# Optimization experiments

Hardware: AMD Instinct MI355X
Metric: run time of the kernel (lower is better)

Reference implementation:

```python
import jax, jax.numpy as jnp
import numpy as np

C = 256
HEADS = 8
HD = C // HEADS
EPS = 1e-5


def _layernorm(x, g, b):
    mu = jnp.mean(x, axis=-1, keepdims=True)
    var = jnp.var(x, axis=-1, keepdims=True)
    return (x - mu) * jax.lax.rsqrt(var + EPS) * g + b


def setup_inputs() -> dict:
    key = jax.random.key(0)
    ks = jax.random.split(key, 16)
    s = 0.02
    return {
        "x": jax.random.normal(ks[0], (1, C, 64, 64), jnp.float32),
        "bn_gamma": 1.0 + s * jax.random.normal(ks[1], (C,), jnp.float32),
        "bn_beta": s * jax.random.normal(ks[2], (C,), jnp.float32),
        "bn_mean": s * jax.random.normal(ks[3], (C,), jnp.float32),
        "bn_var": jnp.ones((C,), jnp.float32),
        "w_in": s * jax.random.normal(ks[4], (C, C), jnp.float32),
        "b_in": jnp.zeros((C,), jnp.float32),
        "ln1_g": jnp.ones((C,), jnp.float32),
        "ln1_b": jnp.zeros((C,), jnp.float32),
        "w_qkv": s * jax.random.normal(ks[5], (3 * C, C), jnp.float32),
        "b_qkv": jnp.zeros((3 * C,), jnp.float32),
        "w_ap": s * jax.random.normal(ks[6], (C, C), jnp.float32),
        "b_ap": jnp.zeros((C,), jnp.float32),
        "ln2_g": jnp.ones((C,), jnp.float32),
        "ln2_b": jnp.zeros((C,), jnp.float32),
        "w_ff1": s * jax.random.normal(ks[7], (4 * C, C), jnp.float32),
        "b_ff1": jnp.zeros((4 * C,), jnp.float32),
        "w_ff2": s * jax.random.normal(ks[8], (C, 4 * C), jnp.float32),
        "b_ff2": jnp.zeros((C,), jnp.float32),
        "w_out": s * jax.random.normal(ks[9], (C, C), jnp.float32),
        "b_out": jnp.zeros((C,), jnp.float32),
    }


def reference(x, bn_gamma, bn_beta, bn_mean, bn_var, w_in, b_in,
              ln1_g, ln1_b, w_qkv, b_qkv, w_ap, b_ap,
              ln2_g, ln2_b, w_ff1, b_ff1, w_ff2, b_ff2, w_out, b_out):
    b, c, h, w = x.shape
    t = h * w
    x_in = x
    # BatchNorm2d (eval mode: running stats)
    xn = (x - bn_mean[None, :, None, None]) * jax.lax.rsqrt(bn_var + EPS)[None, :, None, None]
    xn = xn * bn_gamma[None, :, None, None] + bn_beta[None, :, None, None]
    # proj_in 1x1 conv -> tokens [b, t, c]
    tok = xn.reshape(b, c, t).transpose(0, 2, 1)
    tok = tok @ w_in.T + b_in
    # transformer block (depth=1)
    y = _layernorm(tok, ln1_g, ln1_b)  # norm1
    qkv = y @ w_qkv.T + b_qkv  # [b, t, 3c], channel split (3, H, hd)
    qkv = qkv.reshape(b, t, 3, HEADS, HD)
    q = qkv[:, :, 0].transpose(0, 2, 1, 3)  # [b, H, t, hd]
    k = qkv[:, :, 1].transpose(0, 2, 1, 3)
    v = qkv[:, :, 2].transpose(0, 2, 1, 3)
    scale = HD ** (-0.5)
    attn = jax.nn.softmax(jnp.einsum('bhqd,bhkd->bhqk', q, k) * scale, axis=-1)
    o = jnp.einsum('bhqk,bhkd->bhqd', attn, v)  # [b, H, t, hd]
    o = o.transpose(0, 2, 1, 3).reshape(b, t, c)  # channels ordered (H, hd)
    o = o @ w_ap.T + b_ap  # attn proj 1x1
    attn_out = o + y  # VanillaAttention residual adds its (normed) input
    tok = tok + attn_out
    # FFN
    z = _layernorm(tok, ln2_g, ln2_b)
    z = jax.nn.gelu(z @ w_ff1.T + b_ff1, approximate=False)
    tok = tok + (z @ w_ff2.T + b_ff2)
    # back to image, proj_out 1x1, outer residual
    x4 = tok.transpose(0, 2, 1).reshape(b, c, h, w)
    out = jnp.einsum('oc,bchw->bohw', w_out, x4) + b_out[None, :, None, None]
    return out + x_in
```

## Files before the change

### kernel.cpp

```cpp
#include <hip/hip_runtime.h>
#include <math.h>

#define T_TOK 4096
#define C_DIM 256
#define EPSF  1e-5f
#define SC_QL (0.17677669529663687f * 1.4426950408889634f)

typedef short  bf16x8  __attribute__((ext_vector_type(8)));
typedef float  f32x4   __attribute__((ext_vector_type(4)));
typedef ushort ushort8 __attribute__((ext_vector_type(8)));

__device__ __forceinline__ short f2bf(float f) {
    unsigned u = __builtin_bit_cast(unsigned, f);
    unsigned r = (u + 0x7FFFu + ((u >> 16) & 1u)) >> 16;
    return (short)r;
}
__device__ __forceinline__ float bf2f(ushort u) {
    return __builtin_bit_cast(float, ((unsigned)u) << 16);
}
__device__ __forceinline__ unsigned pk_bf16(float a, float b) {
    const unsigned ua = __builtin_bit_cast(unsigned, a) + 0x8000u;
    const unsigned ub = __builtin_bit_cast(unsigned, b) + 0x8000u;
    return __builtin_amdgcn_perm(ub, ua, 0x07060302u);
}
template <int CTRL>
__device__ __forceinline__ float dppf(float x) {
    return __builtin_bit_cast(float,
        __builtin_amdgcn_mov_dpp(__builtin_bit_cast(int, x), CTRL, 0xF, 0xF, true));
}
__device__ __forceinline__ float rowsum16(float x) {
    x += dppf<0xB1>(x);
    x += dppf<0x4E>(x);
    x += dppf<0x141>(x);
    x += dppf<0x140>(x);
    return x;
}
#define MFMA16(a, b, c) __builtin_amdgcn_mfma_f32_16x16x32_bf16(a, b, c, 0, 0, 0)

__global__ __launch_bounds__(256) void prep_kernel(
    const float* __restrict__ w_in, const float* __restrict__ w_qkv,
    const float* __restrict__ w_ap, const float* __restrict__ w_ff1,
    const float* __restrict__ w_ff2, const float* __restrict__ w_out,
    const float* __restrict__ b_qkv, ushort* __restrict__ wbuf,
    float* __restrict__ bqs,
    const float* __restrict__ x, const float* __restrict__ gamma,
    const float* __restrict__ beta, const float* __restrict__ mean,
    const float* __restrict__ var, ushort* __restrict__ tin)
{
    __shared__ float tile[32][33];
    if (blockIdx.x < 896) {
        const int gid = blockIdx.x * 256 + threadIdx.x;
        const int e0 = gid * 4;
        const float* src; int off; float sc = 1.f;
        if (e0 < 65536)       { src = w_in;  off = e0; }
        else if (e0 < 262144) { src = w_qkv; off = e0 - 65536; if (off < 65536) sc = SC_QL; }
        else if (e0 < 327680) { src = w_ap;  off = e0 - 262144; }
        else if (e0 < 589824) { src = w_ff1; off = e0 - 327680; }
        else if (e0 < 851968) { src = w_ff2; off = e0 - 589824; }
        else                  { src = w_out; off = e0 - 851968; }
        const float4 v = *(const float4*)(src + off);
        ushort4 o;
        o.x = (ushort)f2bf(v.x * sc); o.y = (ushort)f2bf(v.y * sc);
        o.z = (ushort)f2bf(v.z * sc); o.w = (ushort)f2bf(v.w * sc);
        *(ushort4*)(wbuf + e0) = o;
        if (gid < 192) {
            const float s2 = (gid < 64) ? SC_QL : 1.f;
            float4 b = ((const float4*)b_qkv)[gid];
            b.x *= s2; b.y *= s2; b.z *= s2; b.w *= s2;
            ((float4*)bqs)[gid] = b;
        }
    } else {
        const int bidx = blockIdx.x - 896;
        const int t0 = (bidx & 127) * 32, c0 = (bidx >> 7) * 32;
        const int tx = threadIdx.x & 31, ty = threadIdx.x >> 5;
#pragma unroll
        for (int i = 0; i < 32; i += 8) {
            const int c = c0 + ty + i;
            const float a = rsqrtf(var[c] + EPSF) * gamma[c];
            const float d = beta[c] - mean[c] * a;
            tile[ty + i][tx] = x[c * T_TOK + t0 + tx] * a + d;
        }
        __syncthreads();
#pragma unroll
        for (int i = 0; i < 32; i += 8) {
            const int t = t0 + ty + i;
            tin[t * C_DIM + c0 + tx] = (ushort)f2bf(tile[tx][ty + i]);
        }
    }
}

__global__ __launch_bounds__(1024) void fused_pre(
    const ushort* __restrict__ tin, const ushort* __restrict__ wb_in,
    const float* __restrict__ b_in, const float* __restrict__ ln1_g,
    const float* __restrict__ ln1_b, const ushort* __restrict__ wb_qkv,
    const float* __restrict__ bqs, float* __restrict__ tok0,
    float* __restrict__ yout, ushort* __restrict__ qkvb)
{
    __shared__ ushort Atile[16 * 264];
    __shared__ ushort Ytile[16 * 264];
    __shared__ float  red[16][16][2];
    const int t0 = blockIdx.x * 16;
    const int tid = threadIdx.x, wv = tid >> 6, lane = tid & 63;
    const int c = lane & 15, g = lane >> 4;

    {
        const int r = tid >> 6, c0 = (tid & 63) * 4;
        *(ushort4*)&Atile[r * 264 + c0] = *(const ushort4*)(tin + (size_t)(t0 + r) * 256 + c0);
    }
    __syncthreads();

    f32x4 accp = {};
#pragma unroll
    for (int kc = 0; kc < 8; ++kc) {
        const bf16x8 af = *(const bf16x8*)&Atile[c * 264 + kc * 32 + g * 8];
        const bf16x8 bfv = *(const bf16x8*)(wb_in +
            (size_t)(wv * 16 + c) * 256 + kc * 32 + g * 8);
        accp = MFMA16(af, bfv, accp);
    }
    const int colp = wv * 16 + c;
    {
        const float bb = b_in[colp];
        float vs[4], s1[4], s2[4];
#pragma unroll
        for (int rr = 0; rr < 4; ++rr) {
            const float v = accp[rr] + bb;
            vs[rr] = v; s1[rr] = v; s2[rr] = v * v;
            tok0[(size_t)(t0 + 4 * g + rr) * 256 + colp] = v;
        }
#pragma unroll
        for (int rr = 0; rr < 4; ++rr) { s1[rr] = rowsum16(s1[rr]); s2[rr] = rowsum16(s2[rr]); }
        if (c == 0) {
#pragma unroll
            for (int rr = 0; rr < 4; ++rr) {
                red[wv][4 * g + rr][0] = s1[rr];
                red[wv][4 * g + rr][1] = s2[rr];
            }
        }
        __syncthreads();
        if (tid < 32) {
            const int row = tid >> 1, j = tid & 1;
            float s = 0.f;
#pragma unroll
            for (int w = 0; w < 16; ++w) s += red[w][row][j];
            red[0][row][j] = s;
        }
        __syncthreads();
        const float gg = ln1_g[colp], lb = ln1_b[colp];
#pragma unroll
        for (int rr = 0; rr < 4; ++rr) {
            const int row = 4 * g + rr;
            const float mu = red[0][row][0] * (1.0f / 256.0f);
            const float var = red[0][row][1] * (1.0f / 256.0f) - mu * mu;
            const float rs = rsqrtf(var + EPSF);
            const float yv = (vs[rr] - mu) * rs * gg + lb;
            yout[(size_t)(t0 + row) * 256 + colp] = yv;
            Ytile[row * 264 + colp] = (ushort)f2bf(yv);
        }
    }
    __syncthreads();

    f32x4 accq[3] = {};
#pragma unroll
    for (int kc = 0; kc < 8; ++kc) {
        const bf16x8 af = *(const bf16x8*)&Ytile[c * 264 + kc * 32 + g * 8];
#pragma unroll
        for (int nf = 0; nf < 3; ++nf) {
            const bf16x8 bfv = *(const bf16x8*)(wb_qkv +
                (size_t)(wv * 48 + nf * 16 + c) * 256 + kc * 32 + g * 8);
            accq[nf] = MFMA16(af, bfv, accq[nf]);
        }
    }
#pragma unroll
    for (int nf = 0; nf < 3; ++nf) {
        const int col = wv * 48 + nf * 16 + c;
        const float bb = bqs[col];
#pragma unroll
        for (int rr = 0; rr < 4; ++rr)
            qkvb[(size_t)(t0 + 4 * g + rr) * 768 + col] = (ushort)f2bf(accq[nf][rr] + bb);
    }
}

#define KS   40
#define VTS  72
#define PS_W 36

__global__ __launch_bounds__(256) void attn_mfma(
    const ushort* __restrict__ qkv, ushort* __restrict__ o1,
    ushort* __restrict__ o2, float* __restrict__ lpart)
{
    const int h    = blockIdx.y;
    const int q0   = blockIdx.x << 6;
    const int half = blockIdx.z;
    const int tid  = threadIdx.x;
    const int wv   = tid >> 6, lane = tid & 63;
    const int c    = lane & 15, g = lane >> 4;

    __shared__ ushort Ks[2][64 * KS];
    __shared__ ushort Vt[2][32 * VTS];
    __shared__ float  Ps[4][16 * PS_W];

    const bf16x8 qf = *(const bf16x8*)(qkv + (size_t)(q0 + wv * 16 + c) * 768 + h * 32 + g * 8);

    bf16x8 ones;
#pragma unroll
    for (int i = 0; i < 8; ++i) ones[i] = (short)0x3F80;

    f32x4 oacc0 = {0.f, 0.f, 0.f, 0.f};
    f32x4 oacc1 = {0.f, 0.f, 0.f, 0.f};
    f32x4 oaccl = {0.f, 0.f, 0.f, 0.f};

    const int kr = tid >> 2, kc = (tid & 3) * 8;
    const int vp = tid & 31, vd = (tid >> 5) * 4;
    const ushort* kbase = qkv + 256 + h * 32;
    const ushort* vbase = qkv + 512 + h * 32;

    const int kt0 = half * 32, kt1 = kt0 + 32;
    ushort8 kpre  = *(const ushort8*)(kbase + ((size_t)kt0 * 64 + kr) * 768 + kc);
    ushort4 vpre0 = *(const ushort4*)(vbase + ((size_t)kt0 * 64 + 2 * vp) * 768 + vd);
    ushort4 vpre1 = *(const ushort4*)(vbase + ((size_t)kt0 * 64 + 2 * vp + 1) * 768 + vd);

    int p = 0;
    for (int kt = kt0; kt < kt1; ++kt) {
        *(ushort8*)&Ks[p][kr * KS + kc] = kpre;
        {
            unsigned* vtp = (unsigned*)&Vt[p][0];
            vtp[(vd + 0) * (VTS / 2) + vp] = (unsigned)vpre0.x | ((unsigned)vpre1.x << 16);
            vtp[(vd + 1) * (VTS / 2) + vp] = (unsigned)vpre0.y | ((unsigned)vpre1.y << 16);
            vtp[(vd + 2) * (VTS / 2) + vp] = (unsigned)vpre0.z | ((unsigned)vpre1.z << 16);
            vtp[(vd + 3) * (VTS / 2) + vp] = (unsigned)vpre0.w | ((unsigned)vpre1.w << 16);
        }
        __syncthreads();
        if (kt + 1 < kt1) {
            const size_t t0 = (size_t)(kt + 1) * 64;
            kpre  = *(const ushort8*)(kbase + (t0 + kr) * 768 + kc);
            vpre0 = *(const ushort4*)(vbase + (t0 + 2 * vp) * 768 + vd);
            vpre1 = *(const ushort4*)(vbase + (t0 + 2 * vp + 1) * 768 + vd);
        }

        const ushort* ks = &Ks[p][0];
        const ushort* vt = &Vt[p][0];
        const f32x4 zz = {0.f, 0.f, 0.f, 0.f};
        const bf16x8 k0 = *(const bf16x8*)&ks[(0 * 16 + c) * KS + g * 8];
        const bf16x8 k1 = *(const bf16x8*)&ks[(1 * 16 + c) * KS + g * 8];
        const bf16x8 k2 = *(const bf16x8*)&ks[(2 * 16 + c) * KS + g * 8];
        const bf16x8 k3 = *(const bf16x8*)&ks[(3 * 16 + c) * KS + g * 8];
        const f32x4 s0 = MFMA16(k0, qf, zz);
        const f32x4 s1 = MFMA16(k1, qf, zz);
        const f32x4 s2 = MFMA16(k2, qf, zz);
        const f32x4 s3 = MFMA16(k3, qf, zz);

        float* prow = &Ps[wv][c * PS_W];
        {
            const float e00 = __builtin_amdgcn_exp2f(s0[0]), e01 = __builtin_amdgcn_exp2f(s0[1]);
            const float e02 = __builtin_amdgcn_exp2f(s0[2]), e03 = __builtin_amdgcn_exp2f(s0[3]);
            const float e10 = __builtin_amdgcn_exp2f(s1[0]), e11 = __builtin_amdgcn_exp2f(s1[1]);
            const float e12 = __builtin_amdgcn_exp2f(s1[2]), e13 = __builtin_amdgcn_exp2f(s1[3]);
            const float e20 = __builtin_amdgcn_exp2f(s2[0]), e21 = __builtin_amdgcn_exp2f(s2[1]);
            const float e22 = __builtin_amdgcn_exp2f(s2[2]), e23 = __builtin_amdgcn_exp2f(s2[3]);
            const float e30 = __builtin_amdgcn_exp2f(s3[0]), e31 = __builtin_amdgcn_exp2f(s3[1]);
            const float e32 = __builtin_amdgcn_exp2f(s3[2]), e33 = __builtin_amdgcn_exp2f(s3[3]);
            prow[0 * 8 + 2 * g + 0] = __builtin_bit_cast(float, pk_bf16(e00, e01));
            prow[0 * 8 + 2 * g + 1] = __builtin_bit_cast(float, pk_bf16(e02, e03));
            prow[1 * 8 + 2 * g + 0] = __builtin_bit_cast(float, pk_bf16(e10, e11));
            prow[1 * 8 + 2 * g + 1] = __builtin_bit_cast(float, pk_bf16(e12, e13));
            prow[2 * 8 + 2 * g + 0] = __builtin_bit_cast(float, pk_bf16(e20, e21));
            prow[2 * 8 + 2 * g + 1] = __builtin_bit_cast(float, pk_bf16(e22, e23));
            prow[3 * 8 + 2 * g + 0] = __builtin_bit_cast(float, pk_bf16(e30, e31));
            prow[3 * 8 + 2 * g + 1] = __builtin_bit_cast(float, pk_bf16(e32, e33));
        }
#pragma unroll
        for (int ch = 0; ch < 2; ++ch) {
            const bf16x8 pf = *(const bf16x8*)&prow[ch * 16 + 4 * g];
            const bf16x8 v0 = *(const bf16x8*)&vt[(c)      * VTS + ch * 32 + g * 8];
            const bf16x8 v1 = *(const bf16x8*)&vt[(16 + c) * VTS + ch * 32 + g * 8];
            oacc0 = MFMA16(pf, v0, oacc0);
            oacc1 = MFMA16(pf, v1, oacc1);
            oaccl = MFMA16(pf, ones, oaccl);
        }
        p ^= 1;
        __syncthreads();
    }

    {
        ushort* op = (half ? o2 : o1) + (size_t)(q0 + wv * 16) * 256 + h * 32;
#pragma unroll
        for (int rr = 0; rr < 4; ++rr) {
            op[(4 * g + rr) * 256 + c]      = (ushort)f2bf(oacc0[rr]);
            op[(4 * g + rr) * 256 + 16 + c] = (ushort)f2bf(oacc1[rr]);
        }
        if (c == 0) {
#pragma unroll
            for (int rr = 0; rr < 4; ++rr)
                lpart[(size_t)(q0 + wv * 16 + 4 * g + rr) * 16 + half * 8 + h] = oaccl[rr];
        }
    }
}

__global__ __launch_bounds__(1024) void fused_mid(
    const ushort* __restrict__ o1, const ushort* __restrict__ o2,
    const float* __restrict__ lpart, const ushort* __restrict__ wb_ap,
    const float* __restrict__ b_ap, const float* __restrict__ yin,
    const float* __restrict__ tok0, const float* __restrict__ ln2_g,
    const float* __restrict__ ln2_b, const ushort* __restrict__ wb_ff1,
    const float* __restrict__ b_ff1, float* __restrict__ tok1,
    ushort* __restrict__ zbuf)
{
    __shared__ ushort Otile[16 * 264];
    __shared__ ushort Ztile[16 * 264];
    __shared__ float  red[16][16][2];
    const int t0 = blockIdx.x * 16;
    const int tid = threadIdx.x, wv = tid >> 6, lane = tid & 63;
    const int c = lane & 15, g = lane >> 4;

    {
        const int r = tid >> 6, c0 = (tid & 63) * 4;
        const int h = (tid & 63) >> 3;
        const float inv = 1.0f / (lpart[(size_t)(t0 + r) * 16 + h] +
                                  lpart[(size_t)(t0 + r) * 16 + 8 + h]);
        const ushort4 a = *(const ushort4*)(o1 + (size_t)(t0 + r) * 256 + c0);
        const ushort4 b = *(const ushort4*)(o2 + (size_t)(t0 + r) * 256 + c0);
        unsigned w[2];
        w[0] = pk_bf16((bf2f(a.x) + bf2f(b.x)) * inv, (bf2f(a.y) + bf2f(b.y)) * inv);
        w[1] = pk_bf16((bf2f(a.z) + bf2f(b.z)) * inv, (bf2f(a.w) + bf2f(b.w)) * inv);
        *(ushort4*)&Otile[r * 264 + c0] = *(ushort4*)w;
    }
    __syncthreads();

    f32x4 accp = {};
#pragma unroll
    for (int kc = 0; kc < 8; ++kc) {
        const bf16x8 af = *(const bf16x8*)&Otile[c * 264 + kc * 32 + g * 8];
        const bf16x8 bfv = *(const bf16x8*)(wb_ap +
            (size_t)(wv * 16 + c) * 256 + kc * 32 + g * 8);
        accp = MFMA16(af, bfv, accp);
    }
    const int colp = wv * 16 + c;
    {
        const float bb = b_ap[colp];
        float vs[4], s1[4], s2[4];
#pragma unroll
        for (int rr = 0; rr < 4; ++rr) {
            const size_t idx = (size_t)(t0 + 4 * g + rr) * 256 + colp;
            const float v = accp[rr] + bb + yin[idx] + tok0[idx];
            vs[rr] = v; s1[rr] = v; s2[rr] = v * v;
            tok1[idx] = v;
        }
#pragma unroll
        for (int rr = 0; rr < 4; ++rr) { s1[rr] = rowsum16(s1[rr]); s2[rr] = rowsum16(s2[rr]); }
        if (c == 0) {
#pragma unroll
            for (int rr = 0; rr < 4; ++rr) {
                red[wv][4 * g + rr][0] = s1[rr];
                red[wv][4 * g + rr][1] = s2[rr];
            }
        }
        __syncthreads();
        if (tid < 32) {
            const int row = tid >> 1, j = tid & 1;
            float s = 0.f;
#pragma unroll
            for (int w = 0; w < 16; ++w) s += red[w][row][j];
            red[0][row][j] = s;
        }
        __syncthreads();
        const float gg = ln2_g[colp], lb = ln2_b[colp];
#pragma unroll
        for (int rr = 0; rr < 4; ++rr) {
            const int row = 4 * g + rr;
            const float mu = red[0][row][0] * (1.0f / 256.0f);
            const float var = red[0][row][1] * (1.0f / 256.0f) - mu * mu;
            const float rs = rsqrtf(var + EPSF);
            const float zv = (vs[rr] - mu) * rs * gg + lb;
            Ztile[row * 264 + colp] = (ushort)f2bf(zv);
        }
    }
    __syncthreads();

    f32x4 accf[4] = {};
#pragma unroll
    for (int kc = 0; kc < 8; ++kc) {
        const bf16x8 af = *(const bf16x8*)&Ztile[c * 264 + kc * 32 + g * 8];
#pragma unroll
        for (int nf = 0; nf < 4; ++nf) {
            const bf16x8 bfv = *(const bf16x8*)(wb_ff1 +
                (size_t)(wv * 64 + nf * 16 + c) * 256 + kc * 32 + g * 8);
            accf[nf] = MFMA16(af, bfv, accf[nf]);
        }
    }
#pragma unroll
    for (int nf = 0; nf < 4; ++nf) {
        const int col = wv * 64 + nf * 16 + c;
        const float bb = b_ff1[col];
#pragma unroll
        for (int rr = 0; rr < 4; ++rr) {
            float v = accf[nf][rr] + bb;
            v = 0.5f * v * (1.0f + erff(v * 0.70710678118654752f));
            zbuf[(size_t)(t0 + 4 * g + rr) * 1024 + col] = (ushort)f2bf(v);
        }
    }
}

__global__ __launch_bounds__(1024) void fused_post(
    const ushort* __restrict__ zbuf, const ushort* __restrict__ wb_ff2,
    const float* __restrict__ b_ff2, const float* __restrict__ tok1,
    const ushort* __restrict__ wb_out, const float* __restrict__ b_out,
    const float* __restrict__ x, float* __restrict__ out)
{
    __shared__ ushort Ztile[16 * 1032];
    __shared__ ushort T2tile[16 * 264];
    const int t0 = blockIdx.x * 16;
    const int tid = threadIdx.x, wv = tid >> 6, lane = tid & 63;
    const int c = lane & 15, g = lane >> 4;

    {
        const int r = tid >> 6, c0 = (tid & 63) * 16;
        *(ushort8*)&Ztile[r * 1032 + c0] =
            *(const ushort8*)(zbuf + (size_t)(t0 + r) * 1024 + c0);
        *(ushort8*)&Ztile[r * 1032 + c0 + 8] =
            *(const ushort8*)(zbuf + (size_t)(t0 + r) * 1024 + c0 + 8);
    }
    __syncthreads();

    f32x4 accf = {};
#pragma unroll
    for (int kc = 0; kc < 32; ++kc) {
        const bf16x8 af = *(const bf16x8*)&Ztile[c * 1032 + kc * 32 + g * 8];
        const bf16x8 bfv = *(const bf16x8*)(wb_ff2 +
            (size_t)(wv * 16 + c) * 1024 + kc * 32 + g * 8);
        accf = MFMA16(af, bfv, accf);
    }
    {
        const int col = wv * 16 + c;
        const float bb = b_ff2[col];
#pragma unroll
        for (int rr = 0; rr < 4; ++rr) {
            const size_t idx = (size_t)(t0 + 4 * g + rr) * 256 + col;
            const float v = accf[rr] + bb + tok1[idx];
            T2tile[(4 * g + rr) * 264 + col] = (ushort)f2bf(v);
        }
    }
    __syncthreads();

    f32x4 acco = {};
#pragma unroll
    for (int kc = 0; kc < 8; ++kc) {
        const bf16x8 bfr = *(const bf16x8*)&T2tile[c * 264 + kc * 32 + g * 8];
        const bf16x8 afr = *(const bf16x8*)(wb_out +
            (size_t)(wv * 16 + c) * 256 + kc * 32 + g * 8);
        acco = MFMA16(afr, bfr, acco);
    }
#pragma unroll
    for (int rr = 0; rr < 4; ++rr) {
        const int och = wv * 16 + 4 * g + rr;
        const size_t idx = (size_t)och * T_TOK + t0 + c;
        out[idx] = acco[rr] + b_out[och] + x[idx];
    }
}

extern "C" void kernel_launch(void* const* d_in, const int* in_sizes, int n_in,
                              void* d_out, int out_size, void* d_ws, size_t ws_size,
                              hipStream_t stream)
{
    const float* x     = (const float*)d_in[0];
    const float* bn_g  = (const float*)d_in[1];
    const float* bn_b  = (const float*)d_in[2];
    const float* bn_m  = (const float*)d_in[3];
    const float* bn_v  = (const float*)d_in[4];
    const float* w_in  = (const float*)d_in[5];
    const float* b_in  = (const float*)d_in[6];
    const float* ln1_g = (const float*)d_in[7];
    const float* ln1_b = (const float*)d_in[8];
    const float* w_qkv = (const float*)d_in[9];
    const float* b_qkv = (const float*)d_in[10];
    const float* w_ap  = (const float*)d_in[11];
    const float* b_ap  = (const float*)d_in[12];
    const float* ln2_g = (const float*)d_in[13];
    const float* ln2_b = (const float*)d_in[14];
    const float* w_ff1 = (const float*)d_in[15];
    const float* b_ff1 = (const float*)d_in[16];
    const float* w_ff2 = (const float*)d_in[17];
    const float* b_ff2 = (const float*)d_in[18];
    const float* w_out = (const float*)d_in[19];
    const float* b_out = (const float*)d_in[20];
    float* out = (float*)d_out;
    float* ws  = (float*)d_ws;

    const size_t MF = 1u << 20;
    float*  tok0   = ws;
    float*  y      = ws + MF;
    float*  tok1   = ws + 2 * MF;
    ushort* qkv_bf = (ushort*)(ws + 3 * MF);
    ushort* zbuf   = (ushort*)(ws + 4 * MF + MF / 2);
    ushort* tin_bf = (ushort*)(ws + 6 * MF + MF / 2);
    ushort* o1p    = tin_bf;
    ushort* o2p    = (ushort*)(ws + 7 * MF);
    float*  lpart  = ws + 7 * MF + MF / 2;
    ushort* wbuf   = (ushort*)(ws + 7 * MF + MF / 2 + 65536);
    const ushort* wb_in  = wbuf;
    const ushort* wb_qkv = wbuf + 65536;
    const ushort* wb_ap  = wbuf + 262144;
    const ushort* wb_ff1 = wbuf + 327680;
    const ushort* wb_ff2 = wbuf + 589824;
    const ushort* wb_out = wbuf + 851968;
    float* bqs = (float*)(wbuf + 917504);

    prep_kernel<<<1920, 256, 0, stream>>>(w_in, w_qkv, w_ap, w_ff1, w_ff2, w_out,
                                          b_qkv, wbuf, bqs,
                                          x, bn_g, bn_b, bn_m, bn_v, tin_bf);
    fused_pre<<<256, 1024, 0, stream>>>(tin_bf, wb_in, b_in, ln1_g, ln1_b,
                                        wb_qkv, bqs, tok0, y, qkv_bf);
    attn_mfma<<<dim3(64, 8, 2), 256, 0, stream>>>(qkv_bf, o1p, o2p, lpart);
    fused_mid<<<256, 1024, 0, stream>>>(o1p, o2p, lpart, wb_ap, b_ap, y, tok0,
                                        ln2_g, ln2_b, wb_ff1, b_ff1, tok1, zbuf);
    fused_post<<<256, 1024, 0, stream>>>(zbuf, wb_ff2, b_ff2, tok1, wb_out, b_out,
                                         x, out);
}
```

Before: 205.0 us.

## Keep attention P in registers via permlane swaps and single-barrier double buffering

The softmax probability tile is no longer staged through shared memory. It is packed with v_cvt_pk_bf16_f32 and rearranged into the MFMA A-operand layout using v_permlane32/16_swap. The K/V double buffer is restructured so the next tile is written to the other buffer during compute, which leaves one barrier per iteration instead of two. This removes LDS round-trips and a sync but depends on the permlane lane mapping being correct on gfx950.

```diff
diff --git a/kernel.cpp b/kernel.cpp
--- a/kernel.cpp
+++ b/kernel.cpp
@@ -9,6 +9,7 @@
 typedef short  bf16x8  __attribute__((ext_vector_type(8)));
 typedef float  f32x4   __attribute__((ext_vector_type(4)));
 typedef ushort ushort8 __attribute__((ext_vector_type(8)));
+typedef unsigned uint4v __attribute__((ext_vector_type(4)));
 
 __device__ __forceinline__ short f2bf(float f) {
     unsigned u = __builtin_bit_cast(unsigned, f);
@@ -22,6 +23,17 @@
     const unsigned ua = __builtin_bit_cast(unsigned, a) + 0x8000u;
     const unsigned ub = __builtin_bit_cast(unsigned, b) + 0x8000u;
     return __builtin_amdgcn_perm(ub, ua, 0x07060302u);
+}
+__device__ __forceinline__ unsigned cvtpk_bf16(float a, float b) {
+    unsigned r;
+    asm("v_cvt_pk_bf16_f32 %0, %1, %2" : "=v"(r) : "v"(a), "v"(b));
+    return r;
+}
+__device__ __forceinline__ void plswap32(unsigned &a, unsigned &b) {
+    asm("v_permlane32_swap_b32 %0, %1" : "+v"(a), "+v"(b));
+}
+__device__ __forceinline__ void plswap16(unsigned &a, unsigned &b) {
+    asm("v_permlane16_swap_b32 %0, %1" : "+v"(a), "+v"(b));
 }
 template <int CTRL>
 __device__ __forceinline__ float dppf(float x) {
@@ -182,7 +194,6 @@
 
 #define KS   40
 #define VTS  72
-#define PS_W 36
 
 __global__ __launch_bounds__(256) void attn_mfma(
     const ushort* __restrict__ qkv, ushort* __restrict__ o1,
@@ -197,7 +208,6 @@
 
     __shared__ ushort Ks[2][64 * KS];
     __shared__ ushort Vt[2][32 * VTS];
-    __shared__ float  Ps[4][16 * PS_W];
 
     const bf16x8 qf = *(const bf16x8*)(qkv + (size_t)(q0 + wv * 16 + c) * 768 + h * 32 + g * 8);
 
@@ -215,67 +225,82 @@
     const ushort* vbase = qkv + 512 + h * 32;
 
     const int kt0 = half * 32, kt1 = kt0 + 32;
-    ushort8 kpre  = *(const ushort8*)(kbase + ((size_t)kt0 * 64 + kr) * 768 + kc);
-    ushort4 vpre0 = *(const ushort4*)(vbase + ((size_t)kt0 * 64 + 2 * vp) * 768 + vd);
-    ushort4 vpre1 = *(const ushort4*)(vbase + ((size_t)kt0 * 64 + 2 * vp + 1) * 768 + vd);
+
+    {
+        const ushort8 kv  = *(const ushort8*)(kbase + ((size_t)kt0 * 64 + kr) * 768 + kc);
+        const ushort4 va = *(const ushort4*)(vbase + ((size_t)kt0 * 64 + 2 * vp) * 768 + vd);
+        const ushort4 vb = *(const ushort4*)(vbase + ((size_t)kt0 * 64 + 2 * vp + 1) * 768 + vd);
+        *(ushort8*)&Ks[0][kr * KS + kc] = kv;
+        unsigned* vtp = (unsigned*)&Vt[0][0];
+        vtp[(vd + 0) * (VTS / 2) + vp] = (unsigned)va.x | ((unsigned)vb.x << 16);
+        vtp[(vd + 1) * (VTS / 2) + vp] = (unsigned)va.y | ((unsigned)vb.y << 16);
+        vtp[(vd + 2) * (VTS / 2) + vp] = (unsigned)va.z | ((unsigned)vb.z << 16);
+        vtp[(vd + 3) * (VTS / 2) + vp] = (unsigned)va.w | ((unsigned)vb.w << 16);
+    }
+    ushort8 kpre  = *(const ushort8*)(kbase + ((size_t)(kt0 + 1) * 64 + kr) * 768 + kc);
+    ushort4 vpre0 = *(const ushort4*)(vbase + ((size_t)(kt0 + 1) * 64 + 2 * vp) * 768 + vd);
+    ushort4 vpre1 = *(const ushort4*)(vbase + ((size_t)(kt0 + 1) * 64 + 2 * vp + 1) * 768 + vd);
+    __syncthreads();
 
     int p = 0;
     for (int kt = kt0; kt < kt1; ++kt) {
-        *(ushort8*)&Ks[p][kr * KS + kc] = kpre;
-        {
-            unsigned* vtp = (unsigned*)&Vt[p][0];
+        const ushort* ks = &Ks[p][0];
+        const ushort* vt = &Vt[p][0];
+        const bf16x8 k0 = *(const bf16x8*)&ks[(0 * 16 + c) * KS + g * 8];
+        const bf16x8 k1 = *(const bf16x8*)&ks[(1 * 16 + c) * KS + g * 8];
+        const bf16x8 k2 = *(const bf16x8*)&ks[(2 * 16 + c) * KS + g * 8];
+        const bf16x8 k3 = *(const bf16x8*)&ks[(3 * 16 + c) * KS + g * 8];
+
+        if (kt + 1 < kt1) {
+            *(ushort8*)&Ks[p ^ 1][kr * KS + kc] = kpre;
+            unsigned* vtp = (unsigned*)&Vt[p ^ 1][0];
             vtp[(vd + 0) * (VTS / 2) + vp] = (unsigned)vpre0.x | ((unsigned)vpre1.x << 16);
             vtp[(vd + 1) * (VTS / 2) + vp] = (unsigned)vpre0.y | ((unsigned)vpre1.y << 16);
             vtp[(vd + 2) * (VTS / 2) + vp] = (unsigned)vpre0.z | ((unsigned)vpre1.z << 16);
             vtp[(vd + 3) * (VTS / 2) + vp] = (unsigned)vpre0.w | ((unsigned)vpre1.w << 16);
-        }
-        __syncthreads();
-        if (kt + 1 < kt1) {
-            const size_t t0 = (size_t)(kt + 1) * 64;
-            kpre  = *(const ushort8*)(kbase + (t0 + kr) * 768 + kc);
-            vpre0 = *(const ushort4*)(vbase + (t0 + 2 * vp) * 768 + vd);
-            vpre1 = *(const ushort4*)(vbase + (t0 + 2 * vp + 1) * 768 + vd);
-        }
-
-        const ushort* ks = &Ks[p][0];
-        const ushort* vt = &Vt[p][0];
+            if (kt + 2 < kt1) {
+                const size_t t2 = (size_t)(kt + 2) * 64;
+                kpre  = *(const ushort8*)(kbase + (t2 + kr) * 768 + kc);
+                vpre0 = *(const ushort4*)(vbase + (t2 + 2 * vp) * 768 + vd);
+                vpre1 = *(const ushort4*)(vbase + (t2 + 2 * vp + 1) * 768 + vd);
+            }
+        }
+
         const f32x4 zz = {0.f, 0.f, 0.f, 0.f};
-        const bf16x8 k0 = *(const bf16x8*)&ks[(0 * 16 + c) * KS + g * 8];
-        const bf16x8 k1 = *(const bf16x8*)&ks[(1 * 16 + c) * KS + g * 8];
-        const bf16x8 k2 = *(const bf16x8*)&ks[(2 * 16 + c) * KS + g * 8];
-        const bf16x8 k3 = *(const bf16x8*)&ks[(3 * 16 + c) * KS + g * 8];
         const f32x4 s0 = MFMA16(k0, qf, zz);
         const f32x4 s1 = MFMA16(k1, qf, zz);
         const f32x4 s2 = MFMA16(k2, qf, zz);
         const f32x4 s3 = MFMA16(k3, qf, zz);
 
-        float* prow = &Ps[wv][c * PS_W];
+        unsigned w00 = cvtpk_bf16(__builtin_amdgcn_exp2f(s0[0]), __builtin_amdgcn_exp2f(s0[1]));
+        unsigned w01 = cvtpk_bf16(__builtin_amdgcn_exp2f(s0[2]), __builtin_amdgcn_exp2f(s0[3]));
+        unsigned w10 = cvtpk_bf16(__builtin_amdgcn_exp2f(s1[0]), __builtin_amdgcn_exp2f(s1[1]));
+        unsigned w11 = cvtpk_bf16(__builtin_amdgcn_exp2f(s1[2]), __builtin_amdgcn_exp2f(s1[3]));
+        unsigned w20 = cvtpk_bf16(__builtin_amdgcn_exp2f(s2[0]), __builtin_amdgcn_exp2f(s2[1]));
+        unsigned w21 = cvtpk_bf16(__builtin_amdgcn_exp2f(s2[2]), __builtin_amdgcn_exp2f(s2[3]));
+        unsigned w30 = cvtpk_bf16(__builtin_amdgcn_exp2f(s3[0]), __builtin_amdgcn_exp2f(s3[1]));
+        unsigned w31 = cvtpk_bf16(__builtin_amdgcn_exp2f(s3[2]), __builtin_amdgcn_exp2f(s3[3]));
+
+        plswap32(w00, w10); plswap16(w00, w10);
+        plswap32(w01, w11); plswap16(w01, w11);
+        plswap32(w20, w30); plswap16(w20, w30);
+        plswap32(w21, w31); plswap16(w21, w31);
+        const uint4v u0 = {w00, w01, w10, w11};
+        const uint4v u1 = {w20, w21, w30, w31};
+        const bf16x8 pa0 = __builtin_bit_cast(bf16x8, u0);
+        const bf16x8 pa1 = __builtin_bit_cast(bf16x8, u1);
+
         {
-            const float e00 = __builtin_amdgcn_exp2f(s0[0]), e01 = __builtin_amdgcn_exp2f(s0[1]);
-            const float e02 = __builtin_amdgcn_exp2f(s0[2]), e03 = __builtin_amdgcn_exp2f(s0[3]);
-            const float e10 = __builtin_amdgcn_exp2f(s1[0]), e11 = __builtin_amdgcn_exp2f(s1[1]);
-            const float e12 = __builtin_amdgcn_exp2f(s1[2]), e13 = __builtin_amdgcn_exp2f(s1[3]);
-            const float e20 = __builtin_amdgcn_exp2f(s2[0]), e21 = __builtin_amdgcn_exp2f(s2[1]);
-            const float e22 = __builtin_amdgcn_exp2f(s2[2]), e23 = __builtin_amdgcn_exp2f(s2[3]);
-            const float e30 = __builtin_amdgcn_exp2f(s3[0]), e31 = __builtin_amdgcn_exp2f(s3[1]);
-            const float e32 = __builtin_amdgcn_exp2f(s3[2]), e33 = __builtin_amdgcn_exp2f(s3[3]);
-            prow[0 * 8 + 2 * g + 0] = __builtin_bit_cast(float, pk_bf16(e00, e01));
-            prow[0 * 8 + 2 * g + 1] = __builtin_bit_cast(float, pk_bf16(e02, e03));
-            prow[1 * 8 + 2 * g + 0] = __builtin_bit_cast(float, pk_bf16(e10, e11));
-            prow[1 * 8 + 2 * g + 1] = __builtin_bit_cast(float, pk_bf16(e12, e13));
-            prow[2 * 8 + 2 * g + 0] = __builtin_bit_cast(float, pk_bf16(e20, e21));
-            prow[2 * 8 + 2 * g + 1] = __builtin_bit_cast(float, pk_bf16(e22, e23));
-            prow[3 * 8 + 2 * g + 0] = __builtin_bit_cast(float, pk_bf16(e30, e31));
-            prow[3 * 8 + 2 * g + 1] = __builtin_bit_cast(float, pk_bf16(e32, e33));
-        }
-#pragma unroll
-        for (int ch = 0; ch < 2; ++ch) {
-            const bf16x8 pf = *(const bf16x8*)&prow[ch * 16 + 4 * g];
-            const bf16x8 v0 = *(const bf16x8*)&vt[(c)      * VTS + ch * 32 + g * 8];
-            const bf16x8 v1 = *(const bf16x8*)&vt[(16 + c) * VTS + ch * 32 + g * 8];
-            oacc0 = MFMA16(pf, v0, oacc0);
-            oacc1 = MFMA16(pf, v1, oacc1);
-            oaccl = MFMA16(pf, ones, oaccl);
+            const bf16x8 va0 = *(const bf16x8*)&vt[(c)      * VTS + 0 * 32 + g * 8];
+            const bf16x8 vb0 = *(const bf16x8*)&vt[(16 + c) * VTS + 0 * 32 + g * 8];
+            oacc0 = MFMA16(pa0, va0, oacc0);
+            oacc1 = MFMA16(pa0, vb0, oacc1);
+            oaccl = MFMA16(pa0, ones, oaccl);
+            const bf16x8 va1 = *(const bf16x8*)&vt[(c)      * VTS + 1 * 32 + g * 8];
+            const bf16x8 vb1 = *(const bf16x8*)&vt[(16 + c) * VTS + 1 * 32 + g * 8];
+            oacc0 = MFMA16(pa1, va1, oacc0);
+            oacc1 = MFMA16(pa1, vb1, oacc1);
+            oaccl = MFMA16(pa1, ones, oaccl);
         }
         p ^= 1;
         __syncthreads();
```

New measurement: 204.6 us. Within noise of the previous version (-0.2%).
